# Kernel tuning notes

Measured on AMD Instinct MI355X. Metric: run time of the kernel, lower is better.

The kernel has to match this reference:

```python
import jax, jax.numpy as jnp
import numpy as np

N, D, K = 500000, 128, 16

def _glorot(key, shape):
    lim = np.sqrt(6.0 / (shape[0] + shape[-1]))
    return jax.random.uniform(key, shape, jnp.float32, -lim, lim)

def setup_inputs() -> dict:
    key = jax.random.key(0)
    k1, k2, kV, kW, kU = jax.random.split(key, 5)
    x1 = jax.random.normal(k1, (N, D), jnp.float32)
    x2 = jax.random.normal(k2, (1, D), jnp.float32)
    V = _glorot(kV, (K, 2 * D))
    W = _glorot(kW, (K, D, D))
    b = jnp.zeros((K,), jnp.float32)
    U = _glorot(kU, (K, 1))
    return {"x1": x1, "x2": x2, "V": V, "W": W, "b": b, "U": U}

def reference(x1, x2, V, W, b, U):
    # V-term: concat([x1, tile(x2)]) @ V[i]^T, vectorized over K by splitting V.
    d = x1.shape[1]
    v_term = x1 @ V[:, :d].T + x2 @ V[:, d:].T            # (N,K) + (1,K)
    # W-term: (x1 @ W[i]) @ x2^T for each i == x1 @ (W @ x2)^T, vectorized.
    wx2 = jnp.einsum('kde,e->kd', W, x2[0])               # (K,D)
    w_term = x1 @ wx2.T                                   # (N,K)
    out = jax.nn.relu(v_term + w_term + b)                # (N,K)
    return out @ U                                        # (N,1)
```

## Files before the change

### kernel.cpp

```cpp
#include <hip/hip_runtime.h>
#include <hip/hip_bf16.h>


#define D 128
#define KK 16

typedef __attribute__((ext_vector_type(8))) short bf16x8;
typedef __attribute__((ext_vector_type(4))) float f32x4;

__device__ __forceinline__ unsigned short f2bf(float f) {
    unsigned u = __float_as_uint(f);
    unsigned t = u + 0x7fffu + ((u >> 16) & 1u);
    return (unsigned short)(t >> 16);
}
__device__ __forceinline__ float bf2f(unsigned short s) {
    return __uint_as_float(((unsigned)s) << 16);
}

__global__ __launch_bounds__(256) void ntn_prep(const float* __restrict__ x2,
                                                const float* __restrict__ V,
                                                const float* __restrict__ W,
                                                const float* __restrict__ b,
                                                unsigned short* __restrict__ bh,
                                                unsigned short* __restrict__ bl,
                                                float* __restrict__ c) {
    const int gtid = blockIdx.x * 256 + threadIdx.x;
    const int wave = gtid >> 6;
    const int lane = gtid & 63;
    if (wave >= KK * D + KK) return;

    float p;
    if (wave < KK * D) {
        const int k = wave >> 7, d = wave & (D - 1);
        const float* Wr = W + ((size_t)(k * D + d)) * D;
        p = Wr[lane] * x2[lane] + Wr[lane + 64] * x2[lane + 64];
    } else {
        const int k = wave - KK * D;
        const float* Vr = V + (size_t)k * 2 * D + D;
        p = Vr[lane] * x2[lane] + Vr[lane + 64] * x2[lane + 64];
    }
#pragma unroll
    for (int m = 32; m; m >>= 1) p += __shfl_xor(p, m);

    if (lane == 0) {
        if (wave < KK * D) {
            const int k = wave >> 7, d = wave & (D - 1);
            float Mv = V[(size_t)k * 2 * D + d] + p;
            unsigned short hb = f2bf(Mv);
            unsigned short lb = f2bf(Mv - bf2f(hb));
            const int kb = d >> 5, kk = d & 31;
            const int fl = k | ((kk >> 3) << 4);
            const int idx = kb * 512 + fl * 8 + (kk & 7);
            bh[idx] = hb;
            bl[idx] = lb;
        } else {
            const int k = wave - KK * D;
            c[k] = p + b[k];
        }
    }
}

__device__ __forceinline__ uint2 pack4(const float4& v) {
    union { __hip_bfloat162 h; unsigned u; } a, b;
    a.h = __float22bfloat162_rn(make_float2(v.x, v.y));
    b.h = __float22bfloat162_rn(make_float2(v.z, v.w));
    uint2 r; r.x = a.u; r.y = b.u; return r;
}

__global__ __launch_bounds__(256, 4) void ntn_main(const float* __restrict__ x1,
                                                   const unsigned short* __restrict__ bhp,
                                                   const unsigned short* __restrict__ blp,
                                                   const float* __restrict__ cp,
                                                   const float* __restrict__ Up,
                                                   float* __restrict__ out,
                                                   int NT, int C) {
    __shared__ unsigned char lds[4 * 4096];

    const int t = threadIdx.x;
    const int l = t & 63;
    const int gw = blockIdx.x * 4 + (t >> 6);
    unsigned char* const L = lds + (t >> 6) * 4096;

    bf16x8 Bh[4], Bl[4];
#pragma unroll
    for (int kb = 0; kb < 4; ++kb) {
        Bh[kb] = *(const bf16x8*)(bhp + kb * 512 + l * 8);
        Bl[kb] = *(const bf16x8*)(blp + kb * 512 + l * 8);
    }
    const int m = l & 15;
    const int q = l >> 4;
    const float cl = cp[m];
    const float ul = Up[m];

    const int start = gw * C;
    if (start >= NT) return;
    const int end = (start + C < NT) ? start + C : NT;

    const int wr_r0 = (l >> 5);
    const int wr_cb = (l & 31) * 8;
    int rd_off[4];
#pragma unroll
    for (int kb = 0; kb < 4; ++kb)
        rd_off[kb] = m * 256 + ((kb * 64 + q * 16) ^ ((m & 7) * 16));

    const float4* const f4 = (const float4*)x1;

    {
        float4 g[8];
        const size_t base = (size_t)start * 512 + l;
#pragma unroll
        for (int i = 0; i < 8; ++i) g[i] = f4[base + i * 64];
#pragma unroll
        for (int i = 0; i < 8; ++i) {
            const int r = wr_r0 + 2 * i;
            *(uint2*)(L + r * 256 + (wr_cb ^ ((r & 7) * 16))) = pack4(g[i]);
        }
    }

    for (int i = start; i < end; ++i) {
        const bool has = (i + 1 < end);
        float4 g2[8];
        if (has) {
            const size_t base = (size_t)(i + 1) * 512 + l;
#pragma unroll
            for (int j = 0; j < 8; ++j) g2[j] = f4[base + j * 64];
        }

        f32x4 accA = {0.f, 0.f, 0.f, 0.f};
        f32x4 accB = {0.f, 0.f, 0.f, 0.f};
#pragma unroll
        for (int kb = 0; kb < 4; ++kb) {
            bf16x8 ah = *(const bf16x8*)(L + rd_off[kb]);
            accA = __builtin_amdgcn_mfma_f32_16x16x32_bf16(ah, Bh[kb], accA, 0, 0, 0);
            accB = __builtin_amdgcn_mfma_f32_16x16x32_bf16(ah, Bl[kb], accB, 0, 0, 0);
        }

        {
            float vv[4];
#pragma unroll
            for (int r = 0; r < 4; ++r) {
                float s = accA[r] + accB[r] + cl;
                vv[r] = ul * fmaxf(s, 0.f);
                vv[r] += __shfl_xor(vv[r], 1);
                vv[r] += __shfl_xor(vv[r], 2);
                vv[r] += __shfl_xor(vv[r], 4);
                vv[r] += __shfl_xor(vv[r], 8);
            }
            if (m == 0)
                *(float4*)(out + (size_t)i * 16 + q * 4) =
                    make_float4(vv[0], vv[1], vv[2], vv[3]);
        }

        if (has) {
#pragma unroll
            for (int j = 0; j < 8; ++j) {
                const int r = wr_r0 + 2 * j;
                *(uint2*)(L + r * 256 + (wr_cb ^ ((r & 7) * 16))) = pack4(g2[j]);
            }
        }
    }
}

extern "C" void kernel_launch(void* const* d_in, const int* in_sizes, int n_in,
                              void* d_out, int out_size, void* d_ws, size_t ws_size,
                              hipStream_t stream) {
    const float* x1 = (const float*)d_in[0];
    const float* x2 = (const float*)d_in[1];
    const float* V  = (const float*)d_in[2];
    const float* W  = (const float*)d_in[3];
    const float* b  = (const float*)d_in[4];
    const float* U  = (const float*)d_in[5];
    float* out = (float*)d_out;

    unsigned short* bh = (unsigned short*)d_ws;
    unsigned short* bl = bh + KK * D;
    float* c = (float*)(bl + KK * D);

    const int N = in_sizes[0] / D;
    const int NT = N >> 4;

    ntn_prep<<<516, 256, 0, stream>>>(x2, V, W, b, bh, bl, c);

    const int waves = 1024 * 4;
    const int C = (NT + waves - 1) / waves;
    ntn_main<<<1024, 256, 0, stream>>>(x1, bh, bl, c, U, out, NT, C);
}
```

Before: 360.8 us.

## Replace persistent per-wave tile loop with one tile per wave and nontemporal I/O

The main kernel no longer launches a fixed grid of 1024 blocks where each wave walks a chunk of row tiles with a one-tile prefetch. It now launches one wave per 16-row tile across a much larger grid and drops the min-blocks launch bound. The goal is to hide the latency of streaming x1 with many more resident and queued waves rather than serial software prefetch. x1 loads and output stores use nontemporal builtins to avoid polluting the cache. The cost is that every wave re-fetches the B fragments and constants, and there is more per-block launch overhead.

```diff
diff --git a/kernel.cpp b/kernel.cpp
--- a/kernel.cpp
+++ b/kernel.cpp
@@ -7,6 +7,7 @@
 
 typedef __attribute__((ext_vector_type(8))) short bf16x8;
 typedef __attribute__((ext_vector_type(4))) float f32x4;
+typedef __attribute__((ext_vector_type(4))) float f32x4v;
 
 __device__ __forceinline__ unsigned short f2bf(float f) {
     unsigned u = __float_as_uint(f);
@@ -60,26 +61,27 @@
     }
 }
 
-__device__ __forceinline__ uint2 pack4(const float4& v) {
+__device__ __forceinline__ uint2 pack4(const f32x4v& v) {
     union { __hip_bfloat162 h; unsigned u; } a, b;
     a.h = __float22bfloat162_rn(make_float2(v.x, v.y));
     b.h = __float22bfloat162_rn(make_float2(v.z, v.w));
     uint2 r; r.x = a.u; r.y = b.u; return r;
 }
 
-__global__ __launch_bounds__(256, 4) void ntn_main(const float* __restrict__ x1,
-                                                   const unsigned short* __restrict__ bhp,
-                                                   const unsigned short* __restrict__ blp,
-                                                   const float* __restrict__ cp,
-                                                   const float* __restrict__ Up,
-                                                   float* __restrict__ out,
-                                                   int NT, int C) {
+__global__ __launch_bounds__(256) void ntn_main(const float* __restrict__ x1,
+                                                const unsigned short* __restrict__ bhp,
+                                                const unsigned short* __restrict__ blp,
+                                                const float* __restrict__ cp,
+                                                const float* __restrict__ Up,
+                                                float* __restrict__ out,
+                                                int NT) {
     __shared__ unsigned char lds[4 * 4096];
 
     const int t = threadIdx.x;
     const int l = t & 63;
-    const int gw = blockIdx.x * 4 + (t >> 6);
-    unsigned char* const L = lds + (t >> 6) * 4096;
+    const int wid = t >> 6;
+    const int tile = blockIdx.x * 4 + wid;
+    unsigned char* const L = lds + wid * 4096;
 
     bf16x8 Bh[4], Bl[4];
 #pragma unroll
@@ -92,72 +94,49 @@
     const float cl = cp[m];
     const float ul = Up[m];
 
-    const int start = gw * C;
-    if (start >= NT) return;
-    const int end = (start + C < NT) ? start + C : NT;
+    if (tile >= NT) return;
 
-    const int wr_r0 = (l >> 5);
-    const int wr_cb = (l & 31) * 8;
-    int rd_off[4];
+    f32x4v g[8];
+    {
+        const f32x4v* const f4 = (const f32x4v*)x1 + (size_t)tile * 512 + l;
 #pragma unroll
-    for (int kb = 0; kb < 4; ++kb)
-        rd_off[kb] = m * 256 + ((kb * 64 + q * 16) ^ ((m & 7) * 16));
-
-    const float4* const f4 = (const float4*)x1;
+        for (int j = 0; j < 8; ++j)
+            g[j] = __builtin_nontemporal_load(f4 + j * 64);
+    }
 
     {
-        float4 g[8];
-        const size_t base = (size_t)start * 512 + l;
+        const int wr_r0 = (l >> 5);
+        const int wr_cb = (l & 31) * 8;
 #pragma unroll
-        for (int i = 0; i < 8; ++i) g[i] = f4[base + i * 64];
-#pragma unroll
-        for (int i = 0; i < 8; ++i) {
-            const int r = wr_r0 + 2 * i;
-            *(uint2*)(L + r * 256 + (wr_cb ^ ((r & 7) * 16))) = pack4(g[i]);
+        for (int j = 0; j < 8; ++j) {
+            const int r = wr_r0 + 2 * j;
+            *(uint2*)(L + r * 256 + (wr_cb ^ ((r & 7) * 16))) = pack4(g[j]);
         }
     }
 
-    for (int i = start; i < end; ++i) {
-        const bool has = (i + 1 < end);
-        float4 g2[8];
-        if (has) {
-            const size_t base = (size_t)(i + 1) * 512 + l;
+    f32x4 accA = {0.f, 0.f, 0.f, 0.f};
+    f32x4 accB = {0.f, 0.f, 0.f, 0.f};
 #pragma unroll
-            for (int j = 0; j < 8; ++j) g2[j] = f4[base + j * 64];
-        }
+    for (int kb = 0; kb < 4; ++kb) {
+        const int rd = m * 256 + ((kb * 64 + q * 16) ^ ((m & 7) * 16));
+        bf16x8 ah = *(const bf16x8*)(L + rd);
+        accA = __builtin_amdgcn_mfma_f32_16x16x32_bf16(ah, Bh[kb], accA, 0, 0, 0);
+        accB = __builtin_amdgcn_mfma_f32_16x16x32_bf16(ah, Bl[kb], accB, 0, 0, 0);
+    }
 
-        f32x4 accA = {0.f, 0.f, 0.f, 0.f};
-        f32x4 accB = {0.f, 0.f, 0.f, 0.f};
+    float vv[4];
 #pragma unroll
-        for (int kb = 0; kb < 4; ++kb) {
-            bf16x8 ah = *(const bf16x8*)(L + rd_off[kb]);
-            accA = __builtin_amdgcn_mfma_f32_16x16x32_bf16(ah, Bh[kb], accA, 0, 0, 0);
-            accB = __builtin_amdgcn_mfma_f32_16x16x32_bf16(ah, Bl[kb], accB, 0, 0, 0);
-        }
-
-        {
-            float vv[4];
-#pragma unroll
-            for (int r = 0; r < 4; ++r) {
-                float s = accA[r] + accB[r] + cl;
-                vv[r] = ul * fmaxf(s, 0.f);
-                vv[r] += __shfl_xor(vv[r], 1);
-                vv[r] += __shfl_xor(vv[r], 2);
-                vv[r] += __shfl_xor(vv[r], 4);
-                vv[r] += __shfl_xor(vv[r], 8);
-            }
-            if (m == 0)
-                *(float4*)(out + (size_t)i * 16 + q * 4) =
-                    make_float4(vv[0], vv[1], vv[2], vv[3]);
-        }
-
-        if (has) {
-#pragma unroll
-            for (int j = 0; j < 8; ++j) {
-                const int r = wr_r0 + 2 * j;
-                *(uint2*)(L + r * 256 + (wr_cb ^ ((r & 7) * 16))) = pack4(g2[j]);
-            }
-        }
+    for (int r = 0; r < 4; ++r) {
+        float s = accA[r] + accB[r] + cl;
+        vv[r] = ul * fmaxf(s, 0.f);
+        vv[r] += __shfl_xor(vv[r], 1);
+        vv[r] += __shfl_xor(vv[r], 2);
+        vv[r] += __shfl_xor(vv[r], 4);
+        vv[r] += __shfl_xor(vv[r], 8);
+    }
+    if (m == 0) {
+        f32x4v v = {vv[0], vv[1], vv[2], vv[3]};
+        __builtin_nontemporal_store(v, (f32x4v*)(out + (size_t)tile * 16 + q * 4));
     }
 }
 
@@ -181,7 +160,6 @@
 
     ntn_prep<<<516, 256, 0, stream>>>(x2, V, W, b, bh, bl, c);
 
-    const int waves = 1024 * 4;
-    const int C = (NT + waves - 1) / waves;
-    ntn_main<<<1024, 256, 0, stream>>>(x1, bh, bl, c, U, out, NT, C);
+    const int blocks = (NT + 3) / 4;
+    ntn_main<<<blocks, 256, 0, stream>>>(x1, bh, bl, c, U, out, NT);
 }
```

After: 326.3 us. 1.11x faster.
